# Kernel tuning notes

Measured on AMD Instinct MI355X. Metric: run time of the kernel, lower is better.

The kernel has to match this reference:

```python
import jax, jax.numpy as jnp
import numpy as np

TOP_K = 2  # config.n_expert_per_token


def setup_inputs() -> dict:
    key = jax.random.key(0)
    ks = jax.random.split(key, 5)
    B, T, C, E, F = 2, 2048, 2048, 8, 1024
    scale = 0.02
    return {
        "x": jax.random.normal(ks[0], (B, T, C), jnp.float32),
        "w_router": jax.random.normal(ks[1], (C, E), jnp.float32) * scale,
        "w1": jax.random.normal(ks[2], (E, C, F), jnp.float32) * scale,  # fc_1 (gate proj)
        "w3": jax.random.normal(ks[3], (E, C, F), jnp.float32) * scale,  # fc_2 (up proj)
        "w2": jax.random.normal(ks[4], (E, F, C), jnp.float32) * scale,  # proj (down)
    }


def reference(x, w_router, w1, w3, w2):
    B, T, C = x.shape
    xt = x.reshape(-1, C)                                  # [N, C]
    N = xt.shape[0]
    E = w_router.shape[1]
    # Router: topk logits, softmax over the selected k in fp32
    logits = xt @ w_router                                 # [N, E]
    top_vals, top_idx = jax.lax.top_k(logits, TOP_K)       # [N, k]
    probs = jax.nn.softmax(top_vals.astype(jnp.float32), axis=1).astype(xt.dtype)
    # Per-token per-expert combine weight (0 for unselected experts).
    # topk indices are distinct per token, so scatter-add == scatter-set.
    w = jnp.zeros((N, E), xt.dtype).at[jnp.arange(N)[:, None], top_idx].add(probs)  # [N, E]
    # Dense grouped SwiGLU expert MLPs; zero-weight tokens contribute nothing.
    g = jnp.einsum('nc,ecf->enf', xt, w1)                  # [E, N, F]
    u = jnp.einsum('nc,ecf->enf', xt, w3)                  # [E, N, F]
    h = jax.nn.silu(g) * u                                 # [E, N, F]
    outs = jnp.einsum('enf,efc->enc', h, w2)               # [E, N, C]
    y = jnp.einsum('enc,ne->nc', outs, w)                  # weighted combine
    return y.reshape(B, T, C)
```

## Files before the change

kernel.cpp:

```cpp
#include <hip/hip_runtime.h>
#include <hip/hip_bf16.h>
#include <stdint.h>

#define N_TOK 4096
#define CDIM 2048
#define EXP 8
#define FDIM 1024
#define LDSTRIDE 40

typedef __attribute__((ext_vector_type(4))) float f32x4;
typedef __attribute__((ext_vector_type(8))) short bf16x8;

__global__ __launch_bounds__(256) void transpose_to_bf16(
    const float* __restrict__ in, __hip_bfloat16* __restrict__ out, int R, int Cc) {
  __shared__ float tile[64][65];
  int e = blockIdx.z;
  const float* ip = in + (size_t)e * R * Cc;
  __hip_bfloat16* op = out + (size_t)e * R * Cc;
  int r0 = blockIdx.y * 64, c0 = blockIdx.x * 64;
  int t = threadIdx.x;
  {
    int r = t >> 2, cb = (t & 3) * 16;
    const float* src = ip + (size_t)(r0 + r) * Cc + c0 + cb;
#pragma unroll
    for (int i = 0; i < 4; i++) {
      float4 v = *(const float4*)(src + i * 4);
      tile[cb + i * 4 + 0][r] = v.x;
      tile[cb + i * 4 + 1][r] = v.y;
      tile[cb + i * 4 + 2][r] = v.z;
      tile[cb + i * 4 + 3][r] = v.w;
    }
  }
  __syncthreads();
  {
    int c = t >> 2, sb = (t & 3) * 16;
    union { int4 v[2]; __hip_bfloat16 h[16]; } u;
#pragma unroll
    for (int j = 0; j < 16; j++) u.h[j] = __float2bfloat16(tile[c][sb + j]);
    __hip_bfloat16* dst = op + (size_t)(c0 + c) * R + r0 + sb;
    *(int4*)(dst) = u.v[0];
    *(int4*)(dst + 8) = u.v[1];
  }
}

__global__ __launch_bounds__(256) void router_kernel(
    const float* __restrict__ x, const float* __restrict__ wr,
    __hip_bfloat16* __restrict__ x_bf, int* __restrict__ counts,
    int* __restrict__ pair_expert, float* __restrict__ pair_prob) {
  int tok = blockIdx.x;
  const float* xr = x + (size_t)tok * CDIM;
  int t = threadIdx.x;
  float acc[EXP];
#pragma unroll
  for (int e = 0; e < EXP; e++) acc[e] = 0.f;
#pragma unroll
  for (int j = 0; j < 8; j++) {
    int c = j * 256 + t;
    float xv = xr[c];
    x_bf[(size_t)tok * CDIM + c] = __float2bfloat16(xv);
    const float4* wr4 = (const float4*)(wr + (size_t)c * EXP);
    float4 wa = wr4[0], wb = wr4[1];
    acc[0] += xv * wa.x; acc[1] += xv * wa.y; acc[2] += xv * wa.z; acc[3] += xv * wa.w;
    acc[4] += xv * wb.x; acc[5] += xv * wb.y; acc[6] += xv * wb.z; acc[7] += xv * wb.w;
  }
#pragma unroll
  for (int e = 0; e < EXP; e++) {
#pragma unroll
    for (int off = 32; off > 0; off >>= 1) acc[e] += __shfl_down(acc[e], off, 64);
  }
  __shared__ float wsum[4][EXP];
  int wid = t >> 6, lane = t & 63;
  if (lane == 0) {
#pragma unroll
    for (int e = 0; e < EXP; e++) wsum[wid][e] = acc[e];
  }
  __syncthreads();
  if (t == 0) {
    float lg[EXP];
#pragma unroll
    for (int e = 0; e < EXP; e++) lg[e] = wsum[0][e] + wsum[1][e] + wsum[2][e] + wsum[3][e];
    int i0 = 0;
#pragma unroll
    for (int e = 1; e < EXP; e++) if (lg[e] > lg[i0]) i0 = e;
    int i1 = (i0 == 0) ? 1 : 0;
#pragma unroll
    for (int e = 0; e < EXP; e++) if (e != i0 && lg[e] > lg[i1]) i1 = e;
    float e1 = __expf(lg[i1] - lg[i0]);
    float p0 = 1.f / (1.f + e1);
    pair_expert[tok * 2 + 0] = i0;
    pair_expert[tok * 2 + 1] = i1;
    pair_prob[tok * 2 + 0] = p0;
    pair_prob[tok * 2 + 1] = e1 * p0;
    atomicAdd(&counts[i0], 1);
    atomicAdd(&counts[i1], 1);
  }
}

__global__ void scan_kernel(const int* __restrict__ counts, int* __restrict__ bases) {
  if (threadIdx.x == 0) {
    int s = 0;
    for (int e = 0; e < EXP; e++) { bases[e] = s; s += counts[e]; }
  }
}

__global__ __launch_bounds__(256) void scatter_kernel(
    const int* __restrict__ pair_expert, const int* __restrict__ bases,
    int* __restrict__ cursors, int* __restrict__ lists) {
  int tok = blockIdx.x * 256 + threadIdx.x;
  if (tok >= N_TOK) return;
#pragma unroll
  for (int k = 0; k < 2; k++) {
    int e = pair_expert[tok * 2 + k];
    int pos = atomicAdd(&cursors[e], 1);
    lists[bases[e] + pos] = tok * 2 + k;
  }
}

__global__ __launch_bounds__(256) void gemm1_kernel(
    const __hip_bfloat16* __restrict__ xbf, const __hip_bfloat16* __restrict__ w1t,
    const __hip_bfloat16* __restrict__ w3t, const int* __restrict__ counts,
    const int* __restrict__ bases, const int* __restrict__ lists,
    __hip_bfloat16* __restrict__ h) {
  int e = blockIdx.z;
  int n_e = counts[e];
  int m0 = blockIdx.y * 128;
  if (m0 >= n_e) return;
  int base = bases[e];
  int f0 = blockIdx.x * 64;

  __shared__ short As[128 * LDSTRIDE];
  __shared__ short B1s[64 * LDSTRIDE];
  __shared__ short B3s[64 * LDSTRIDE];

  int t = threadIdx.x;
  int lane = t & 63, wid = t >> 6;

  int arow = t >> 1;
  int achunk = (t & 1) * 16;
  int rr = m0 + arow;
  int pair = lists[base + ((rr < n_e) ? rr : 0)];
  int tokA = pair >> 1;

  const short* xs = (const short*)xbf;
  const short* b1p = (const short*)w1t + (size_t)e * FDIM * CDIM;
  const short* b3p = (const short*)w3t + (size_t)e * FDIM * CDIM;
  int brow = (t & 127) >> 1;
  bool doB1 = (t < 128);
  const short* bsrc = (doB1 ? b1p : b3p) + (size_t)(f0 + brow) * CDIM + achunk;
  short* bdst = (doB1 ? B1s : B3s) + brow * LDSTRIDE + achunk;
  const short* asrc = xs + (size_t)tokA * CDIM + achunk;
  short* adst = As + arow * LDSTRIDE + achunk;

  int4 pa0 = *(const int4*)(asrc);
  int4 pa1 = *(const int4*)(asrc + 8);
  int4 pb0 = *(const int4*)(bsrc);
  int4 pb1 = *(const int4*)(bsrc + 8);

  f32x4 zero = {0.f, 0.f, 0.f, 0.f};
  f32x4 accg[4][2], accu[4][2];
#pragma unroll
  for (int i = 0; i < 4; i++)
#pragma unroll
    for (int j = 0; j < 2; j++) { accg[i][j] = zero; accu[i][j] = zero; }

  int wm = (wid & 1) * 64, wf = (wid >> 1) * 32;
  int kq = (lane >> 4) * 8;
  int rsel = lane & 15;

  for (int kk = 0; kk < CDIM; kk += 32) {
    __syncthreads();
    *(int4*)(adst) = pa0;
    *(int4*)(adst + 8) = pa1;
    *(int4*)(bdst) = pb0;
    *(int4*)(bdst + 8) = pb1;
    __syncthreads();
    if (kk + 32 < CDIM) {
      pa0 = *(const int4*)(asrc + kk + 32);
      pa1 = *(const int4*)(asrc + kk + 40);
      pb0 = *(const int4*)(bsrc + kk + 32);
      pb1 = *(const int4*)(bsrc + kk + 40);
    }
    bf16x8 af[4], b1f[2], b3f[2];
#pragma unroll
    for (int i = 0; i < 4; i++)
      af[i] = *(const bf16x8*)(As + (wm + i * 16 + rsel) * LDSTRIDE + kq);
#pragma unroll
    for (int j = 0; j < 2; j++) {
      b1f[j] = *(const bf16x8*)(B1s + (wf + j * 16 + rsel) * LDSTRIDE + kq);
      b3f[j] = *(const bf16x8*)(B3s + (wf + j * 16 + rsel) * LDSTRIDE + kq);
    }
#pragma unroll
    for (int i = 0; i < 4; i++)
#pragma unroll
      for (int j = 0; j < 2; j++) {
        accg[i][j] = __builtin_amdgcn_mfma_f32_16x16x32_bf16(af[i], b1f[j], accg[i][j], 0, 0, 0);
        accu[i][j] = __builtin_amdgcn_mfma_f32_16x16x32_bf16(af[i], b3f[j], accu[i][j], 0, 0, 0);
      }
  }

  int col = lane & 15;
  int rbase = (lane >> 4) * 4;
#pragma unroll
  for (int i = 0; i < 4; i++) {
#pragma unroll
    for (int r = 0; r < 4; r++) {
      int m = m0 + wm + i * 16 + rbase + r;
      if (m < n_e) {
        size_t hrow = (size_t)(base + m) * FDIM;
#pragma unroll
        for (int j = 0; j < 2; j++) {
          int f = f0 + wf + j * 16 + col;
          float g = accg[i][j][r];
          float u = accu[i][j][r];
          float sg = g / (1.f + __expf(-g));
          h[hrow + f] = __float2bfloat16(sg * u);
        }
      }
    }
  }
}

__global__ __launch_bounds__(256) void gemm2_kernel(
    const __hip_bfloat16* __restrict__ h, const __hip_bfloat16* __restrict__ w2t,
    const int* __restrict__ counts, const int* __restrict__ bases,
    const int* __restrict__ lists, const float* __restrict__ pair_prob,
    float* __restrict__ out) {
  int e = blockIdx.z;
  int n_e = counts[e];
  int m0 = blockIdx.y * 128;
  if (m0 >= n_e) return;
  int base = bases[e];
  int c0 = blockIdx.x * 128;

  __shared__ short As[128 * LDSTRIDE];
  __shared__ short Bs[128 * LDSTRIDE];

  int t = threadIdx.x;
  int lane = t & 63, wid = t >> 6;

  int arow = t >> 1;
  int achunk = (t & 1) * 16;
  int hr = base + m0 + arow;
  if (hr > 2 * N_TOK - 1) hr = 2 * N_TOK - 1;
  const short* hp = (const short*)h;
  const short* bp = (const short*)w2t + (size_t)e * CDIM * FDIM;
  const short* asrc = hp + (size_t)hr * FDIM + achunk;
  const short* bsrc = bp + (size_t)(c0 + arow) * FDIM + achunk;
  short* adst = As + arow * LDSTRIDE + achunk;
  short* bdst = Bs + arow * LDSTRIDE + achunk;

  int4 pa0 = *(const int4*)(asrc);
  int4 pa1 = *(const int4*)(asrc + 8);
  int4 pb0 = *(const int4*)(bsrc);
  int4 pb1 = *(const int4*)(bsrc + 8);

  f32x4 zero = {0.f, 0.f, 0.f, 0.f};
  f32x4 acc[4][4];
#pragma unroll
  for (int i = 0; i < 4; i++)
#pragma unroll
    for (int j = 0; j < 4; j++) acc[i][j] = zero;

  int wm = (wid & 1) * 64, wn = (wid >> 1) * 64;
  int kq = (lane >> 4) * 8;
  int rsel = lane & 15;

  for (int kk = 0; kk < FDIM; kk += 32) {
    __syncthreads();
    *(int4*)(adst) = pa0;
    *(int4*)(adst + 8) = pa1;
    *(int4*)(bdst) = pb0;
    *(int4*)(bdst + 8) = pb1;
    __syncthreads();
    if (kk + 32 < FDIM) {
      pa0 = *(const int4*)(asrc + kk + 32);
      pa1 = *(const int4*)(asrc + kk + 40);
      pb0 = *(const int4*)(bsrc + kk + 32);
      pb1 = *(const int4*)(bsrc + kk + 40);
    }
    bf16x8 af[4], bfr[4];
#pragma unroll
    for (int i = 0; i < 4; i++)
      af[i] = *(const bf16x8*)(As + (wm + i * 16 + rsel) * LDSTRIDE + kq);
#pragma unroll
    for (int j = 0; j < 4; j++)
      bfr[j] = *(const bf16x8*)(Bs + (wn + j * 16 + rsel) * LDSTRIDE + kq);
#pragma unroll
    for (int i = 0; i < 4; i++)
#pragma unroll
      for (int j = 0; j < 4; j++)
        acc[i][j] = __builtin_amdgcn_mfma_f32_16x16x32_bf16(af[i], bfr[j], acc[i][j], 0, 0, 0);
  }

  int col = lane & 15;
  int rbase = (lane >> 4) * 4;
#pragma unroll
  for (int i = 0; i < 4; i++) {
#pragma unroll
    for (int r = 0; r < 4; r++) {
      int m = m0 + wm + i * 16 + rbase + r;
      if (m < n_e) {
        int pr = lists[base + m];
        int tok = pr >> 1;
        float p = pair_prob[pr];
        size_t orow = (size_t)tok * CDIM;
#pragma unroll
        for (int j = 0; j < 4; j++) {
          int c = c0 + wn + j * 16 + col;
          atomicAdd(&out[orow + c], acc[i][j][r] * p);
        }
      }
    }
  }
}

extern "C" void kernel_launch(void* const* d_in, const int* in_sizes, int n_in,
                              void* d_out, int out_size, void* d_ws, size_t ws_size,
                              hipStream_t stream) {
  const float* x  = (const float*)d_in[0];
  const float* wr = (const float*)d_in[1];
  const float* w1 = (const float*)d_in[2];
  const float* w3 = (const float*)d_in[3];
  const float* w2 = (const float*)d_in[4];
  float* out = (float*)d_out;

  char* ws = (char*)d_ws;
  __hip_bfloat16* x_bf = (__hip_bfloat16*)(ws);
  __hip_bfloat16* h    = (__hip_bfloat16*)(ws + 16777216);
  __hip_bfloat16* w1t  = (__hip_bfloat16*)(ws + 33554432);
  __hip_bfloat16* w3t  = (__hip_bfloat16*)(ws + 67108864);
  __hip_bfloat16* w2t  = (__hip_bfloat16*)(ws + 100663296);
  int* counts  = (int*)(ws + 134217728);
  int* bases   = counts + 8;
  int* cursors = counts + 16;
  int* pair_expert = (int*)(ws + 134217728 + 128);
  float* pair_prob = (float*)(ws + 134217728 + 128 + 32768);
  int* lists       = (int*)(ws + 134217728 + 128 + 65536);

  hipMemsetAsync(d_out, 0, (size_t)N_TOK * CDIM * sizeof(float), stream);
  hipMemsetAsync(counts, 0, 128, stream);

  transpose_to_bf16<<<dim3(FDIM / 64, CDIM / 64, EXP), 256, 0, stream>>>(w1, w1t, CDIM, FDIM);
  transpose_to_bf16<<<dim3(FDIM / 64, CDIM / 64, EXP), 256, 0, stream>>>(w3, w3t, CDIM, FDIM);
  transpose_to_bf16<<<dim3(CDIM / 64, FDIM / 64, EXP), 256, 0, stream>>>(w2, w2t, FDIM, CDIM);

  router_kernel<<<N_TOK, 256, 0, stream>>>(x, wr, x_bf, counts, pair_expert, pair_prob);
  scan_kernel<<<1, 64, 0, stream>>>(counts, bases);
  scatter_kernel<<<N_TOK / 256, 256, 0, stream>>>(pair_expert, bases, cursors, lists);

  gemm1_kernel<<<dim3(FDIM / 64, N_TOK / 128, EXP), 256, 0, stream>>>(
      x_bf, w1t, w3t, counts, bases, lists, h);
  gemm2_kernel<<<dim3(CDIM / 128, N_TOK / 128, EXP), 256, 0, stream>>>(
      h, w2t, counts, bases, lists, pair_prob, out);
}
```

Baseline: 625.8 us.

## Replace atomic scatter-add with per-pair output buffer and combine kernel, deepen K tile

The router prob is folded into the gemm1 epilogue so h is pre-scaled. gemm2 now writes bf16 per-pair rows into a reused workspace region (the w1t slot) instead of doing fp32 atomicAdds into the output. A new combine kernel sums each token's two rows through an inverse slot map, which also removes the output memset. Both GEMMs double their K tile from 32 to 64 with a padded LDS stride, halving barriers per K, and the router's bf16 conversion of x is vectorized. The cost is an extra bf16 rounding of per-expert outputs and one more kernel launch.

```diff
diff --git a/kernel.cpp b/kernel.cpp
--- a/kernel.cpp
+++ b/kernel.cpp
@@ -6,7 +6,7 @@
 #define CDIM 2048
 #define EXP 8
 #define FDIM 1024
-#define LDSTRIDE 40
+#define LDK 72
 
 typedef __attribute__((ext_vector_type(4))) float f32x4;
 typedef __attribute__((ext_vector_type(8))) short bf16x8;
@@ -57,11 +57,21 @@
   for (int j = 0; j < 8; j++) {
     int c = j * 256 + t;
     float xv = xr[c];
-    x_bf[(size_t)tok * CDIM + c] = __float2bfloat16(xv);
     const float4* wr4 = (const float4*)(wr + (size_t)c * EXP);
     float4 wa = wr4[0], wb = wr4[1];
     acc[0] += xv * wa.x; acc[1] += xv * wa.y; acc[2] += xv * wa.z; acc[3] += xv * wa.w;
     acc[4] += xv * wb.x; acc[5] += xv * wb.y; acc[6] += xv * wb.z; acc[7] += xv * wb.w;
+  }
+  {
+    int c8 = t * 8;
+    float4 v0 = *(const float4*)(xr + c8);
+    float4 v1 = *(const float4*)(xr + c8 + 4);
+    union { int4 q; __hip_bfloat16 hh[8]; } u;
+    u.hh[0] = __float2bfloat16(v0.x); u.hh[1] = __float2bfloat16(v0.y);
+    u.hh[2] = __float2bfloat16(v0.z); u.hh[3] = __float2bfloat16(v0.w);
+    u.hh[4] = __float2bfloat16(v1.x); u.hh[5] = __float2bfloat16(v1.y);
+    u.hh[6] = __float2bfloat16(v1.z); u.hh[7] = __float2bfloat16(v1.w);
+    *(int4*)(x_bf + (size_t)tok * CDIM + c8) = u.q;
   }
 #pragma unroll
   for (int e = 0; e < EXP; e++) {
@@ -105,14 +115,16 @@
 
 __global__ __launch_bounds__(256) void scatter_kernel(
     const int* __restrict__ pair_expert, const int* __restrict__ bases,
-    int* __restrict__ cursors, int* __restrict__ lists) {
+    int* __restrict__ cursors, int* __restrict__ lists, int* __restrict__ inv) {
   int tok = blockIdx.x * 256 + threadIdx.x;
   if (tok >= N_TOK) return;
 #pragma unroll
   for (int k = 0; k < 2; k++) {
     int e = pair_expert[tok * 2 + k];
     int pos = atomicAdd(&cursors[e], 1);
-    lists[bases[e] + pos] = tok * 2 + k;
+    int slot = bases[e] + pos;
+    lists[slot] = tok * 2 + k;
+    inv[tok * 2 + k] = slot;
   }
 }
 
@@ -120,7 +132,7 @@
     const __hip_bfloat16* __restrict__ xbf, const __hip_bfloat16* __restrict__ w1t,
     const __hip_bfloat16* __restrict__ w3t, const int* __restrict__ counts,
     const int* __restrict__ bases, const int* __restrict__ lists,
-    __hip_bfloat16* __restrict__ h) {
+    const float* __restrict__ pair_prob, __hip_bfloat16* __restrict__ h) {
   int e = blockIdx.z;
   int n_e = counts[e];
   int m0 = blockIdx.y * 128;
@@ -128,15 +140,15 @@
   int base = bases[e];
   int f0 = blockIdx.x * 64;
 
-  __shared__ short As[128 * LDSTRIDE];
-  __shared__ short B1s[64 * LDSTRIDE];
-  __shared__ short B3s[64 * LDSTRIDE];
+  __shared__ short As[128 * LDK];
+  __shared__ short B1s[64 * LDK];
+  __shared__ short B3s[64 * LDK];
 
   int t = threadIdx.x;
   int lane = t & 63, wid = t >> 6;
 
   int arow = t >> 1;
-  int achunk = (t & 1) * 16;
+  int achunk = (t & 1) * 32;
   int rr = m0 + arow;
   int pair = lists[base + ((rr < n_e) ? rr : 0)];
   int tokA = pair >> 1;
@@ -147,14 +159,16 @@
   int brow = (t & 127) >> 1;
   bool doB1 = (t < 128);
   const short* bsrc = (doB1 ? b1p : b3p) + (size_t)(f0 + brow) * CDIM + achunk;
-  short* bdst = (doB1 ? B1s : B3s) + brow * LDSTRIDE + achunk;
+  short* bdst = (doB1 ? B1s : B3s) + brow * LDK + achunk;
   const short* asrc = xs + (size_t)tokA * CDIM + achunk;
-  short* adst = As + arow * LDSTRIDE + achunk;
-
-  int4 pa0 = *(const int4*)(asrc);
-  int4 pa1 = *(const int4*)(asrc + 8);
-  int4 pb0 = *(const int4*)(bsrc);
-  int4 pb1 = *(const int4*)(bsrc + 8);
+  short* adst = As + arow * LDK + achunk;
+
+  int4 pa[4], pb[4];
+#pragma unroll
+  for (int q = 0; q < 4; q++) {
+    pa[q] = *(const int4*)(asrc + q * 8);
+    pb[q] = *(const int4*)(bsrc + q * 8);
+  }
 
   f32x4 zero = {0.f, 0.f, 0.f, 0.f};
   f32x4 accg[4][2], accu[4][2];
@@ -167,35 +181,41 @@
   int kq = (lane >> 4) * 8;
   int rsel = lane & 15;
 
-  for (int kk = 0; kk < CDIM; kk += 32) {
+  for (int kk = 0; kk < CDIM; kk += 64) {
     __syncthreads();
-    *(int4*)(adst) = pa0;
-    *(int4*)(adst + 8) = pa1;
-    *(int4*)(bdst) = pb0;
-    *(int4*)(bdst + 8) = pb1;
+#pragma unroll
+    for (int q = 0; q < 4; q++) {
+      *(int4*)(adst + q * 8) = pa[q];
+      *(int4*)(bdst + q * 8) = pb[q];
+    }
     __syncthreads();
-    if (kk + 32 < CDIM) {
-      pa0 = *(const int4*)(asrc + kk + 32);
-      pa1 = *(const int4*)(asrc + kk + 40);
-      pb0 = *(const int4*)(bsrc + kk + 32);
-      pb1 = *(const int4*)(bsrc + kk + 40);
-    }
-    bf16x8 af[4], b1f[2], b3f[2];
-#pragma unroll
-    for (int i = 0; i < 4; i++)
-      af[i] = *(const bf16x8*)(As + (wm + i * 16 + rsel) * LDSTRIDE + kq);
-#pragma unroll
-    for (int j = 0; j < 2; j++) {
-      b1f[j] = *(const bf16x8*)(B1s + (wf + j * 16 + rsel) * LDSTRIDE + kq);
-      b3f[j] = *(const bf16x8*)(B3s + (wf + j * 16 + rsel) * LDSTRIDE + kq);
-    }
-#pragma unroll
-    for (int i = 0; i < 4; i++)
+    if (kk + 64 < CDIM) {
+#pragma unroll
+      for (int q = 0; q < 4; q++) {
+        pa[q] = *(const int4*)(asrc + kk + 64 + q * 8);
+        pb[q] = *(const int4*)(bsrc + kk + 64 + q * 8);
+      }
+    }
+#pragma unroll
+    for (int hh = 0; hh < 2; hh++) {
+      int kq2 = hh * 32 + kq;
+      bf16x8 af[4], b1f[2], b3f[2];
+#pragma unroll
+      for (int i = 0; i < 4; i++)
+        af[i] = *(const bf16x8*)(As + (wm + i * 16 + rsel) * LDK + kq2);
 #pragma unroll
       for (int j = 0; j < 2; j++) {
-        accg[i][j] = __builtin_amdgcn_mfma_f32_16x16x32_bf16(af[i], b1f[j], accg[i][j], 0, 0, 0);
-        accu[i][j] = __builtin_amdgcn_mfma_f32_16x16x32_bf16(af[i], b3f[j], accu[i][j], 0, 0, 0);
+        b1f[j] = *(const bf16x8*)(B1s + (wf + j * 16 + rsel) * LDK + kq2);
+        b3f[j] = *(const bf16x8*)(B3s + (wf + j * 16 + rsel) * LDK + kq2);
       }
+#pragma unroll
+      for (int i = 0; i < 4; i++)
+#pragma unroll
+        for (int j = 0; j < 2; j++) {
+          accg[i][j] = __builtin_amdgcn_mfma_f32_16x16x32_bf16(af[i], b1f[j], accg[i][j], 0, 0, 0);
+          accu[i][j] = __builtin_amdgcn_mfma_f32_16x16x32_bf16(af[i], b3f[j], accu[i][j], 0, 0, 0);
+        }
+    }
   }
 
   int col = lane & 15;
@@ -206,6 +226,8 @@
     for (int r = 0; r < 4; r++) {
       int m = m0 + wm + i * 16 + rbase + r;
       if (m < n_e) {
+        int pr = lists[base + m];
+        float p = pair_prob[pr];
         size_t hrow = (size_t)(base + m) * FDIM;
 #pragma unroll
         for (int j = 0; j < 2; j++) {
@@ -213,7 +235,7 @@
           float g = accg[i][j][r];
           float u = accu[i][j][r];
           float sg = g / (1.f + __expf(-g));
-          h[hrow + f] = __float2bfloat16(sg * u);
+          h[hrow + f] = __float2bfloat16(p * sg * u);
         }
       }
     }
@@ -223,8 +245,7 @@
 __global__ __launch_bounds__(256) void gemm2_kernel(
     const __hip_bfloat16* __restrict__ h, const __hip_bfloat16* __restrict__ w2t,
     const int* __restrict__ counts, const int* __restrict__ bases,
-    const int* __restrict__ lists, const float* __restrict__ pair_prob,
-    float* __restrict__ out) {
+    __hip_bfloat16* __restrict__ o_pair) {
   int e = blockIdx.z;
   int n_e = counts[e];
   int m0 = blockIdx.y * 128;
@@ -232,27 +253,29 @@
   int base = bases[e];
   int c0 = blockIdx.x * 128;
 
-  __shared__ short As[128 * LDSTRIDE];
-  __shared__ short Bs[128 * LDSTRIDE];
+  __shared__ short As[128 * LDK];
+  __shared__ short Bs[128 * LDK];
 
   int t = threadIdx.x;
   int lane = t & 63, wid = t >> 6;
 
   int arow = t >> 1;
-  int achunk = (t & 1) * 16;
+  int achunk = (t & 1) * 32;
   int hr = base + m0 + arow;
   if (hr > 2 * N_TOK - 1) hr = 2 * N_TOK - 1;
   const short* hp = (const short*)h;
   const short* bp = (const short*)w2t + (size_t)e * CDIM * FDIM;
   const short* asrc = hp + (size_t)hr * FDIM + achunk;
   const short* bsrc = bp + (size_t)(c0 + arow) * FDIM + achunk;
-  short* adst = As + arow * LDSTRIDE + achunk;
-  short* bdst = Bs + arow * LDSTRIDE + achunk;
-
-  int4 pa0 = *(const int4*)(asrc);
-  int4 pa1 = *(const int4*)(asrc + 8);
-  int4 pb0 = *(const int4*)(bsrc);
-  int4 pb1 = *(const int4*)(bsrc + 8);
+  short* adst = As + arow * LDK + achunk;
+  short* bdst = Bs + arow * LDK + achunk;
+
+  int4 pa[4], pb[4];
+#pragma unroll
+  for (int q = 0; q < 4; q++) {
+    pa[q] = *(const int4*)(asrc + q * 8);
+    pb[q] = *(const int4*)(bsrc + q * 8);
+  }
 
   f32x4 zero = {0.f, 0.f, 0.f, 0.f};
   f32x4 acc[4][4];
@@ -265,31 +288,37 @@
   int kq = (lane >> 4) * 8;
   int rsel = lane & 15;
 
-  for (int kk = 0; kk < FDIM; kk += 32) {
+  for (int kk = 0; kk < FDIM; kk += 64) {
     __syncthreads();
-    *(int4*)(adst) = pa0;
-    *(int4*)(adst + 8) = pa1;
-    *(int4*)(bdst) = pb0;
-    *(int4*)(bdst + 8) = pb1;
+#pragma unroll
+    for (int q = 0; q < 4; q++) {
+      *(int4*)(adst + q * 8) = pa[q];
+      *(int4*)(bdst + q * 8) = pb[q];
+    }
     __syncthreads();
-    if (kk + 32 < FDIM) {
-      pa0 = *(const int4*)(asrc + kk + 32);
-      pa1 = *(const int4*)(asrc + kk + 40);
-      pb0 = *(const int4*)(bsrc + kk + 32);
-      pb1 = *(const int4*)(bsrc + kk + 40);
-    }
-    bf16x8 af[4], bfr[4];
-#pragma unroll
-    for (int i = 0; i < 4; i++)
-      af[i] = *(const bf16x8*)(As + (wm + i * 16 + rsel) * LDSTRIDE + kq);
-#pragma unroll
-    for (int j = 0; j < 4; j++)
-      bfr[j] = *(const bf16x8*)(Bs + (wn + j * 16 + rsel) * LDSTRIDE + kq);
-#pragma unroll
-    for (int i = 0; i < 4; i++)
+    if (kk + 64 < FDIM) {
+#pragma unroll
+      for (int q = 0; q < 4; q++) {
+        pa[q] = *(const int4*)(asrc + kk + 64 + q * 8);
+        pb[q] = *(const int4*)(bsrc + kk + 64 + q * 8);
+      }
+    }
+#pragma unroll
+    for (int hh = 0; hh < 2; hh++) {
+      int kq2 = hh * 32 + kq;
+      bf16x8 af[4], bfr[4];
+#pragma unroll
+      for (int i = 0; i < 4; i++)
+        af[i] = *(const bf16x8*)(As + (wm + i * 16 + rsel) * LDK + kq2);
 #pragma unroll
       for (int j = 0; j < 4; j++)
-        acc[i][j] = __builtin_amdgcn_mfma_f32_16x16x32_bf16(af[i], bfr[j], acc[i][j], 0, 0, 0);
+        bfr[j] = *(const bf16x8*)(Bs + (wn + j * 16 + rsel) * LDK + kq2);
+#pragma unroll
+      for (int i = 0; i < 4; i++)
+#pragma unroll
+        for (int j = 0; j < 4; j++)
+          acc[i][j] = __builtin_amdgcn_mfma_f32_16x16x32_bf16(af[i], bfr[j], acc[i][j], 0, 0, 0);
+    }
   }
 
   int col = lane & 15;
@@ -300,18 +329,40 @@
     for (int r = 0; r < 4; r++) {
       int m = m0 + wm + i * 16 + rbase + r;
       if (m < n_e) {
-        int pr = lists[base + m];
-        int tok = pr >> 1;
-        float p = pair_prob[pr];
-        size_t orow = (size_t)tok * CDIM;
+        size_t orow = (size_t)(base + m) * CDIM;
 #pragma unroll
         for (int j = 0; j < 4; j++) {
           int c = c0 + wn + j * 16 + col;
-          atomicAdd(&out[orow + c], acc[i][j][r] * p);
+          o_pair[orow + c] = __float2bfloat16(acc[i][j][r]);
         }
       }
     }
   }
+}
+
+__global__ __launch_bounds__(256) void combine_kernel(
+    const __hip_bfloat16* __restrict__ o_pair, const int* __restrict__ inv,
+    float* __restrict__ out) {
+  int tok = blockIdx.x;
+  int t = threadIdx.x;
+  int s0 = inv[tok * 2], s1 = inv[tok * 2 + 1];
+  const short* p0 = (const short*)o_pair + (size_t)s0 * CDIM + t * 8;
+  const short* p1 = (const short*)o_pair + (size_t)s1 * CDIM + t * 8;
+  union { int4 q; __hip_bfloat16 hh[8]; } a, b;
+  a.q = *(const int4*)p0;
+  b.q = *(const int4*)p1;
+  float* op = out + (size_t)tok * CDIM + t * 8;
+  float4 r0, r1;
+  r0.x = __bfloat162float(a.hh[0]) + __bfloat162float(b.hh[0]);
+  r0.y = __bfloat162float(a.hh[1]) + __bfloat162float(b.hh[1]);
+  r0.z = __bfloat162float(a.hh[2]) + __bfloat162float(b.hh[2]);
+  r0.w = __bfloat162float(a.hh[3]) + __bfloat162float(b.hh[3]);
+  r1.x = __bfloat162float(a.hh[4]) + __bfloat162float(b.hh[4]);
+  r1.y = __bfloat162float(a.hh[5]) + __bfloat162float(b.hh[5]);
+  r1.z = __bfloat162float(a.hh[6]) + __bfloat162float(b.hh[6]);
+  r1.w = __bfloat162float(a.hh[7]) + __bfloat162float(b.hh[7]);
+  *(float4*)(op) = r0;
+  *(float4*)(op + 4) = r1;
 }
 
 extern "C" void kernel_launch(void* const* d_in, const int* in_sizes, int n_in,
@@ -330,14 +381,15 @@
   __hip_bfloat16* w1t  = (__hip_bfloat16*)(ws + 33554432);
   __hip_bfloat16* w3t  = (__hip_bfloat16*)(ws + 67108864);
   __hip_bfloat16* w2t  = (__hip_bfloat16*)(ws + 100663296);
+  __hip_bfloat16* o_pair = w1t;
   int* counts  = (int*)(ws + 134217728);
   int* bases   = counts + 8;
   int* cursors = counts + 16;
   int* pair_expert = (int*)(ws + 134217728 + 128);
   float* pair_prob = (float*)(ws + 134217728 + 128 + 32768);
   int* lists       = (int*)(ws + 134217728 + 128 + 65536);
-
-  hipMemsetAsync(d_out, 0, (size_t)N_TOK * CDIM * sizeof(float), stream);
+  int* inv         = (int*)(ws + 134217728 + 128 + 98304);
+
   hipMemsetAsync(counts, 0, 128, stream);
 
   transpose_to_bf16<<<dim3(FDIM / 64, CDIM / 64, EXP), 256, 0, stream>>>(w1, w1t, CDIM, FDIM);
@@ -346,10 +398,11 @@
 
   router_kernel<<<N_TOK, 256, 0, stream>>>(x, wr, x_bf, counts, pair_expert, pair_prob);
   scan_kernel<<<1, 64, 0, stream>>>(counts, bases);
-  scatter_kernel<<<N_TOK / 256, 256, 0, stream>>>(pair_expert, bases, cursors, lists);
+  scatter_kernel<<<N_TOK / 256, 256, 0, stream>>>(pair_expert, bases, cursors, lists, inv);
 
   gemm1_kernel<<<dim3(FDIM / 64, N_TOK / 128, EXP), 256, 0, stream>>>(
-      x_bf, w1t, w3t, counts, bases, lists, h);
+      x_bf, w1t, w3t, counts, bases, lists, pair_prob, h);
   gemm2_kernel<<<dim3(CDIM / 128, N_TOK / 128, EXP), 256, 0, stream>>>(
-      h, w2t, counts, bases, lists, pair_prob, out);
-}
+      h, w2t, counts, bases, o_pair);
+  combine_kernel<<<N_TOK, 256, 0, stream>>>(o_pair, inv, out);
+}
```

Measured after the change: 1.083 ms. 73.1% more time.
